# Kernel tuning notes

Measured on AMD Instinct MI355X. Metric: run time of the kernel, lower is better.

The kernel has to match this reference:

```python
import jax, jax.numpy as jnp
import numpy as np
import math

B = 16
D = 1024
K = 64
ALPHA = 0.0
N_MAX = 8192


def setup_inputs() -> dict:
    key = jax.random.key(0)
    k1, k2 = jax.random.split(key)
    lengths = jax.random.randint(k1, (B,), N_MAX // 2, N_MAX + 1)
    lengths = lengths.at[0].set(N_MAX)  # ensure max(lengths) == N_MAX, matching torch N_max
    lengths = lengths.astype(jnp.int64) if jax.config.jax_enable_x64 else lengths.astype(jnp.int32)
    W = jax.random.normal(k2, (D, 2 * K), dtype=jnp.float32) * (1.0 / math.sqrt(2 * K))
    return {"lengths": lengths, "W": W, "N_max": N_MAX}


def reference(lengths, W, N_max):
    # lengths: [B] int, W: [d, 2K] (torch Linear weight), N_max: python int
    d, twoK = W.shape
    Kk = twoK // 2
    k = jnp.arange(1, Kk + 1, dtype=jnp.float32)                      # [K]
    Delta = 2.0 * math.pi * k[None, :] / lengths[:, None].astype(jnp.float32)  # [B, K]
    t = jnp.arange(N_max, dtype=jnp.float32)                          # [N]
    theta = t[None, :, None] * Delta[:, None, :]                      # [B, N, K] closed-form angle
    amp = (k ** (-ALPHA)) * (1.0 / math.sqrt(Kk))                     # [K]
    # interleave (cos, sin) pairs along last dim: [c1,s1,c2,s2,...]
    cs = jnp.stack([jnp.cos(theta), jnp.sin(theta)], axis=-1)         # [B, N, K, 2]
    feats = (cs * amp[None, None, :, None]).reshape(theta.shape[0], N_max, twoK)
    mask = jnp.arange(N_max)[None, :] < lengths[:, None]              # [B, N]
    feats = feats * mask[:, :, None].astype(feats.dtype)
    pos_emb = jnp.einsum('bnf,df->bnd', feats, W)                     # [B, N, d]
    return pos_emb, mask
```

## Files before the change

kernel.cpp:

```cpp
#include <hip/hip_runtime.h>
#include <math.h>

#define B_DIM    16
#define D_DIM    1024
#define K_FREQ   64
#define F_DIM    128
#define N_MAXLEN 8192

#define BM   128
#define LDSS 136
#define TILE_SHORTS (128 * LDSS)

typedef __attribute__((ext_vector_type(8))) short bf16x8;
typedef __attribute__((ext_vector_type(4))) float f32x4;

__device__ __forceinline__ unsigned f2bf(float x) {
    union { float f; unsigned u; } v; v.f = x;
    return (v.u + 0x7FFFu + ((v.u >> 16) & 1u)) >> 16;
}

__device__ __forceinline__ void gload_lds16(const void* g, void* l) {
    __builtin_amdgcn_global_load_lds(
        (const __attribute__((address_space(1))) void*)g,
        (__attribute__((address_space(3))) void*)l, 16, 0, 0);
}

__global__ __launch_bounds__(256) void prep_kernel(
    const int* __restrict__ lengths,
    const float* __restrict__ W,
    short* __restrict__ Wb,
    float* __restrict__ maskp)
{
    const int i = blockIdx.x * 256 + threadIdx.x;
    const float4 w = ((const float4*)W)[i];
    const int row = i >> 5;
    const int c4  = i & 31;
    unsigned* p = (unsigned*)&Wb[row * LDSS + c4 * 4];
    p[0] = f2bf(w.x) | (f2bf(w.y) << 16);
    p[1] = f2bf(w.z) | (f2bf(w.w) << 16);

    const int m4  = i << 2;
    const int b   = m4 >> 13;
    const int n   = m4 & (N_MAXLEN - 1);
    const int len = lengths[b];
    float4 mv;
    mv.x = (n     < len) ? 1.f : 0.f;
    mv.y = (n + 1 < len) ? 1.f : 0.f;
    mv.z = (n + 2 < len) ? 1.f : 0.f;
    mv.w = (n + 3 < len) ? 1.f : 0.f;
    ((float4*)maskp)[i] = mv;
}

__global__ __launch_bounds__(256, 3) void cyclic_gemm_kernel(
    const int* __restrict__ lengths,
    const short* __restrict__ Wb,
    float* __restrict__ out)
{
    __shared__ short sB[TILE_SHORTS];

    const int tid  = threadIdx.x;
    const int lane = tid & 63;
    const int wave = tid >> 6;
    const int lrow = lane & 15;
    const int quad = lane >> 4;
    const int m0   = blockIdx.x * BM;
    const int b    = m0 >> 13;
    const int n0   = m0 & (N_MAXLEN - 1);
    const int len  = lengths[b];

    if (n0 >= len) {
        const float4 z = {0.f, 0.f, 0.f, 0.f};
        float4* p = (float4*)(out + (size_t)m0 * D_DIM);
        #pragma unroll 8
        for (int i = tid; i < BM * D_DIM / 4; i += 256) p[i] = z;
        return;
    }

    {
        const short* Wt = Wb;
        #pragma unroll
        for (int i = 0; i < 8; ++i) {
            const int cb = i * 256 + wave * 64;
            gload_lds16(Wt + (size_t)(cb + lane) * 8, sB + (size_t)cb * 8);
        }
        if (wave < 2) {
            const int cb = 2048 + wave * 64;
            gload_lds16(Wt + (size_t)(cb + lane) * 8, sB + (size_t)cb * 8);
        }
    }

    bf16x8 af[2][4];
    #pragma unroll
    for (int mi = 0; mi < 2; ++mi) {
        const int n = n0 + wave * 32 + mi * 16 + lrow;
        if (n >= len) {
            #pragma unroll
            for (int ks = 0; ks < 4; ++ks)
                af[mi][ks] = (bf16x8){0,0,0,0,0,0,0,0};
        } else {
            const float base = (float)n / (float)len;
            #pragma unroll
            for (int ks = 0; ks < 4; ++ks) {
                #pragma unroll
                for (int jj = 0; jj < 4; ++jj) {
                    const int k = ks * 16 + quad * 4 + jj;
                    float rev = base * (float)(k + 1);
                    rev -= floorf(rev);
                    float s, c;
                    __sincosf(6.283185307179586f * rev, &s, &c);
                    af[mi][ks][2*jj]     = (short)f2bf(c * 0.125f);
                    af[mi][ks][2*jj + 1] = (short)f2bf(s * 0.125f);
                }
            }
        }
    }

    #pragma unroll 1
    for (int t = 0; t < 8; ++t) {
        __syncthreads();

        f32x4 acc[2][8];
        #pragma unroll
        for (int mi = 0; mi < 2; ++mi)
            #pragma unroll
            for (int ni = 0; ni < 8; ++ni)
                acc[mi][ni] = (f32x4){0.f, 0.f, 0.f, 0.f};

        #pragma unroll
        for (int ks = 0; ks < 4; ++ks) {
            bf16x8 bfr[8];
            #pragma unroll
            for (int ni = 0; ni < 8; ++ni)
                bfr[ni] = *(const bf16x8*)&sB[(ni*16 + lrow) * LDSS + ks*32 + quad*8];
            #pragma unroll
            for (int mi = 0; mi < 2; ++mi)
                #pragma unroll
                for (int ni = 0; ni < 8; ++ni)
                    acc[mi][ni] = __builtin_amdgcn_mfma_f32_16x16x32_bf16(
                        bfr[ni], af[mi][ks], acc[mi][ni], 0, 0, 0);
        }

        if (t < 7) {
            __syncthreads();
            const short* Wt = Wb + (size_t)(t + 1) * TILE_SHORTS;
            #pragma unroll
            for (int i = 0; i < 8; ++i) {
                const int cb = i * 256 + wave * 64;
                gload_lds16(Wt + (size_t)(cb + lane) * 8, sB + (size_t)cb * 8);
            }
            if (wave < 2) {
                const int cb = 2048 + wave * 64;
                gload_lds16(Wt + (size_t)(cb + lane) * 8, sB + (size_t)cb * 8);
            }
        }

        const int d0 = t * 128;
        #pragma unroll
        for (int mi = 0; mi < 2; ++mi) {
            const int m = m0 + wave * 32 + mi * 16 + lrow;
            float* orow = out + (size_t)m * D_DIM + d0 + quad * 4;
            #pragma unroll
            for (int ni = 0; ni < 8; ++ni)
                *(float4*)(orow + ni * 16) = *(float4*)&acc[mi][ni];
        }
    }
}

extern "C" void kernel_launch(void* const* d_in, const int* in_sizes, int n_in,
                              void* d_out, int out_size, void* d_ws, size_t ws_size,
                              hipStream_t stream) {
    const int*   lengths = (const int*)d_in[0];
    const float* W       = (const float*)d_in[1];
    float* out   = (float*)d_out;
    float* maskp = out + (size_t)B_DIM * N_MAXLEN * D_DIM;
    short* Wb    = (short*)d_ws;

    prep_kernel<<<dim3(128), dim3(256), 0, stream>>>(lengths, W, Wb, maskp);

    dim3 grid((B_DIM * N_MAXLEN) / BM);
    cyclic_gemm_kernel<<<grid, dim3(256), 0, stream>>>(lengths, Wb, out);
}
```

Measured before the change: 545.5 us.

## Load W fragments directly from global memory instead of staging through LDS

```diff
diff --git a/kernel.cpp b/kernel.cpp
--- a/kernel.cpp
+++ b/kernel.cpp
@@ -8,8 +8,6 @@
 #define N_MAXLEN 8192
 
 #define BM   128
-#define LDSS 136
-#define TILE_SHORTS (128 * LDSS)
 
 typedef __attribute__((ext_vector_type(8))) short bf16x8;
 typedef __attribute__((ext_vector_type(4))) float f32x4;
@@ -17,12 +15,6 @@
 __device__ __forceinline__ unsigned f2bf(float x) {
     union { float f; unsigned u; } v; v.f = x;
     return (v.u + 0x7FFFu + ((v.u >> 16) & 1u)) >> 16;
-}
-
-__device__ __forceinline__ void gload_lds16(const void* g, void* l) {
-    __builtin_amdgcn_global_load_lds(
-        (const __attribute__((address_space(1))) void*)g,
-        (__attribute__((address_space(3))) void*)l, 16, 0, 0);
 }
 
 __global__ __launch_bounds__(256) void prep_kernel(
@@ -33,11 +25,10 @@
 {
     const int i = blockIdx.x * 256 + threadIdx.x;
     const float4 w = ((const float4*)W)[i];
-    const int row = i >> 5;
-    const int c4  = i & 31;
-    unsigned* p = (unsigned*)&Wb[row * LDSS + c4 * 4];
-    p[0] = f2bf(w.x) | (f2bf(w.y) << 16);
-    p[1] = f2bf(w.z) | (f2bf(w.w) << 16);
+    uint2 packed;
+    packed.x = f2bf(w.x) | (f2bf(w.y) << 16);
+    packed.y = f2bf(w.z) | (f2bf(w.w) << 16);
+    ((uint2*)Wb)[i] = packed;
 
     const int m4  = i << 2;
     const int b   = m4 >> 13;
@@ -56,8 +47,6 @@
     const short* __restrict__ Wb,
     float* __restrict__ out)
 {
-    __shared__ short sB[TILE_SHORTS];
-
     const int tid  = threadIdx.x;
     const int lane = tid & 63;
     const int wave = tid >> 6;
@@ -74,19 +63,6 @@
         #pragma unroll 8
         for (int i = tid; i < BM * D_DIM / 4; i += 256) p[i] = z;
         return;
-    }
-
-    {
-        const short* Wt = Wb;
-        #pragma unroll
-        for (int i = 0; i < 8; ++i) {
-            const int cb = i * 256 + wave * 64;
-            gload_lds16(Wt + (size_t)(cb + lane) * 8, sB + (size_t)cb * 8);
-        }
-        if (wave < 2) {
-            const int cb = 2048 + wave * 64;
-            gload_lds16(Wt + (size_t)(cb + lane) * 8, sB + (size_t)cb * 8);
-        }
     }
 
     bf16x8 af[2][4];
@@ -115,9 +91,10 @@
         }
     }
 
-    #pragma unroll 1
+    const short* Wlane = Wb + (size_t)lrow * F_DIM + quad * 8;
+    #pragma unroll 2
     for (int t = 0; t < 8; ++t) {
-        __syncthreads();
+        const short* Wt = Wlane + (size_t)t * 128 * F_DIM;
 
         f32x4 acc[2][8];
         #pragma unroll
@@ -131,27 +108,13 @@
             bf16x8 bfr[8];
             #pragma unroll
             for (int ni = 0; ni < 8; ++ni)
-                bfr[ni] = *(const bf16x8*)&sB[(ni*16 + lrow) * LDSS + ks*32 + quad*8];
+                bfr[ni] = *(const bf16x8*)(Wt + (size_t)ni * 16 * F_DIM + ks * 32);
             #pragma unroll
             for (int mi = 0; mi < 2; ++mi)
                 #pragma unroll
                 for (int ni = 0; ni < 8; ++ni)
                     acc[mi][ni] = __builtin_amdgcn_mfma_f32_16x16x32_bf16(
                         bfr[ni], af[mi][ks], acc[mi][ni], 0, 0, 0);
-        }
-
-        if (t < 7) {
-            __syncthreads();
-            const short* Wt = Wb + (size_t)(t + 1) * TILE_SHORTS;
-            #pragma unroll
-            for (int i = 0; i < 8; ++i) {
-                const int cb = i * 256 + wave * 64;
-                gload_lds16(Wt + (size_t)(cb + lane) * 8, sB + (size_t)cb * 8);
-            }
-            if (wave < 2) {
-                const int cb = 2048 + wave * 64;
-                gload_lds16(Wt + (size_t)(cb + lane) * 8, sB + (size_t)cb * 8);
-            }
         }
 
         const int d0 = t * 128;
```

After: 620.1 us. 1.14x slower.
